# Optimization experiments

Hardware: AMD Instinct MI355X
Metric: run time of the kernel (lower is better)

## Reference

```python
import jax, jax.numpy as jnp
import numpy as np


def setup_inputs() -> dict:
    key = jax.random.key(0)
    X = jax.random.normal(key, (8, 64, 64, 64), dtype=jnp.float32)
    return {"X": X}


def reference(X):
    N, C, h, w = X.shape
    x1 = X.reshape(N, C, h * w)            # [N, C, HW]
    x2 = jnp.transpose(x1, (0, 2, 1))      # [N, HW, C]
    scores = jnp.einsum('bnc,bcm->bnm', x2, x1)  # [N, HW, HW]
    c = jax.nn.softmax(scores, axis=2)
    out = jnp.einsum('bnm,bmc->bnc', c, x2)      # [N, HW, C]
    out = jnp.transpose(out, (0, 2, 1)).reshape(N, C, h, w)
    return out
```

## Files before the change

### kernel.cpp

```cpp
#include <hip/hip_runtime.h>


#define SEQ 4096
#define DIM 64
#define LDB 72
#define LDP 72
#define LDO 68

typedef __attribute__((ext_vector_type(8))) short  short8;
typedef __attribute__((ext_vector_type(4))) float  f32x4;

__device__ __forceinline__ unsigned short f2bf(float f) {
    union { float f; unsigned int u; } x; x.f = f;
    unsigned int u = x.u + 0x7FFFu + ((x.u >> 16) & 1u);
    return (unsigned short)(u >> 16);
}
__device__ __forceinline__ float bf2f(unsigned short h) {
    union { unsigned int u; float f; } x; x.u = ((unsigned int)h) << 16; return x.f;
}

__global__ __launch_bounds__(256) void prepass2(const float* __restrict__ X,
                                                unsigned short* __restrict__ Xbf,
                                                unsigned short* __restrict__ XbfT,
                                                float* __restrict__ Norms,
                                                float* __restrict__ MaxNorm) {
    __shared__ float sN[16 * 65];
    const int b = blockIdx.y, m0 = blockIdx.x * 64;
    const float* Xb = X + (size_t)b * DIM * SEQ;
    unsigned short* Bb = Xbf  + (size_t)b * DIM * SEQ;
    unsigned short* Tb = XbfT + (size_t)b * SEQ * DIM;
    const int t = threadIdx.x, mw = t & 15, cg = t >> 4;

    unsigned short hb[4][4];
    #pragma unroll
    for (int cr = 0; cr < 4; ++cr) {
        const int c = cg * 4 + cr;
        const f32x4 v = *(const f32x4*)(Xb + (size_t)c * SEQ + m0 + mw * 4);
        hb[cr][0] = f2bf(v.x); hb[cr][1] = f2bf(v.y); hb[cr][2] = f2bf(v.z); hb[cr][3] = f2bf(v.w);
        *(ushort4*)(Bb + (size_t)c * SEQ + m0 + mw * 4) =
            make_ushort4(hb[cr][0], hb[cr][1], hb[cr][2], hb[cr][3]);
    }
    #pragma unroll
    for (int mr = 0; mr < 4; ++mr) {
        float nrm = 0.f;
        #pragma unroll
        for (int cr = 0; cr < 4; ++cr) { const float fv = bf2f(hb[cr][mr]); nrm += fv * fv; }
        *(ushort4*)(Tb + (size_t)(m0 + mw * 4 + mr) * DIM + cg * 4) =
            make_ushort4(hb[0][mr], hb[1][mr], hb[2][mr], hb[3][mr]);
        sN[cg * 65 + mw * 4 + mr] = nrm;
    }
    __syncthreads();
    if (t < 64) {
        float s = 0.f;
        #pragma unroll
        for (int i = 0; i < 16; ++i) s += sN[i * 65 + t];
        const float nm = sqrtf(s);
        Norms[(size_t)b * SEQ + m0 + t] = nm;
        float mx = nm;
        #pragma unroll
        for (int d = 1; d < 64; d <<= 1) mx = fmaxf(mx, __shfl_xor(mx, d));
        if (t == 0) atomicMax((unsigned int*)(MaxNorm + b), __float_as_uint(mx));
    }
}

__global__ __launch_bounds__(256, 2) void attn_main(const unsigned short* __restrict__ Xbf,
                                                    const unsigned short* __restrict__ XbfT,
                                                    const float* __restrict__ Norms,
                                                    const float* __restrict__ MaxNorm,
                                                    float* __restrict__ Out) {
    __shared__ __align__(16) unsigned char smem[16384 + 16384 + 4 * 16 * LDP * 2];
    unsigned short* sK = (unsigned short*)smem;
    unsigned short* sV = (unsigned short*)(smem + 16384);
    unsigned short* sP = (unsigned short*)(smem + 32768);
    float*          sO = (float*)smem;

    const int tid  = threadIdx.x;
    const int lane = tid & 63;
    const int w    = tid >> 6;
    const int l15  = lane & 15;
    const int quad = lane >> 4;

    const int b  = blockIdx.y;
    const int s0 = blockIdx.x * 64;
    const unsigned short* Bb = Xbf  + (size_t)b * DIM * SEQ;
    const unsigned short* Tb = XbfT + (size_t)b * SEQ * DIM;

    const unsigned short* qp = Tb + (size_t)(s0 + 16 * w + l15) * DIM + quad * 8;
    const short8 qf0 = *(const short8*)(qp);
    const short8 qf1 = *(const short8*)(qp + 32);

    const float mrow = Norms[(size_t)b * SEQ + s0 + 16 * w + l15] * MaxNorm[b];

    f32x4 acc_o[4];
    #pragma unroll
    for (int ct = 0; ct < 4; ++ct) acc_o[ct] = (f32x4){0.f, 0.f, 0.f, 0.f};
    float lpart = 0.f;
    unsigned short* sPw = sP + w * 16 * LDP;

    const int rl = lane >> 3, cgp = lane & 7;
    const int cgs = cgp ^ rl;
    auto stage = [&](int kt, int half) {
        unsigned short* sKb = sK + half * 4096;
        unsigned short* sVb = sV + half * 4096;
        #pragma unroll
        for (int j = 0; j < 2; ++j) {
            const int row = (2 * w + j) * 8 + rl;
            const unsigned short* gK = Tb + ((size_t)(kt * 64 + row) << 6) + (cgs << 3);
            const unsigned short* gV = Bb + (((size_t)row) << 12) + (kt << 6) + (cgs << 3);
            __builtin_amdgcn_global_load_lds(
                (const __attribute__((address_space(1))) unsigned int*)gK,
                (__attribute__((address_space(3))) unsigned int*)(sKb + ((2 * w + j) << 9)),
                16, 0, 0);
            __builtin_amdgcn_global_load_lds(
                (const __attribute__((address_space(1))) unsigned int*)gV,
                (__attribute__((address_space(3))) unsigned int*)(sVb + ((2 * w + j) << 9)),
                16, 0, 0);
        }
    };

    const int rsw = l15 & 7;
    auto compute = [&](int half) {
        const unsigned short* sKc = sK + half * 4096;
        const unsigned short* sVc = sV + half * 4096;
        short8 kf[2][4], vf[2][4];
        #pragma unroll
        for (int t4 = 0; t4 < 4; ++t4) {
            const int rowoff = (16 * t4 + l15) << 6;
            #pragma unroll
            for (int ks = 0; ks < 2; ++ks) {
                const int cgr = (((quad + 4 * ks) ^ rsw) << 3);
                kf[ks][t4] = *(const short8*)(sKc + rowoff + cgr);
                vf[ks][t4] = *(const short8*)(sVc + rowoff + cgr);
            }
        }
        #pragma unroll
        for (int mt = 0; mt < 4; ++mt) {
            f32x4 a = (f32x4){0.f, 0.f, 0.f, 0.f};
            a = __builtin_amdgcn_mfma_f32_16x16x32_bf16(kf[0][mt], qf0, a, 0, 0, 0);
            a = __builtin_amdgcn_mfma_f32_16x16x32_bf16(kf[1][mt], qf1, a, 0, 0, 0);
            const float p0 = __expf(a[0] - mrow);
            const float p1 = __expf(a[1] - mrow);
            const float p2 = __expf(a[2] - mrow);
            const float p3 = __expf(a[3] - mrow);
            lpart += (p0 + p1) + (p2 + p3);
            const unsigned u0 = __float_as_uint(p0) + 0x8000u;
            const unsigned u1 = __float_as_uint(p1) + 0x8000u;
            const unsigned u2 = __float_as_uint(p2) + 0x8000u;
            const unsigned u3 = __float_as_uint(p3) + 0x8000u;
            const unsigned lo = __builtin_amdgcn_perm(u1, u0, 0x07060302u);
            const unsigned hi = __builtin_amdgcn_perm(u3, u2, 0x07060302u);
            *(uint2*)(sPw + l15 * LDP + 16 * mt + quad * 4) = make_uint2(lo, hi);
        }
        const short8 pf0 = *(const short8*)(sPw + l15 * LDP + quad * 8);
        const short8 pf1 = *(const short8*)(sPw + l15 * LDP + 32 + quad * 8);
        #pragma unroll
        for (int ct = 0; ct < 4; ++ct) {
            acc_o[ct] = __builtin_amdgcn_mfma_f32_16x16x32_bf16(pf0, vf[0][ct], acc_o[ct], 0, 0, 0);
            acc_o[ct] = __builtin_amdgcn_mfma_f32_16x16x32_bf16(pf1, vf[1][ct], acc_o[ct], 0, 0, 0);
        }
    };

    stage(0, 0);
    __syncthreads();
    for (int kt = 0; kt < 64; kt += 2) {
        stage(kt + 1, 1);
        compute(0);
        __syncthreads();
        if (kt + 2 < 64) stage(kt + 2, 0);
        compute(1);
        __syncthreads();
    }

    lpart += __shfl_xor(lpart, 16);
    lpart += __shfl_xor(lpart, 32);
    float inv[4];
    #pragma unroll
    for (int r = 0; r < 4; ++r) inv[r] = 1.f / __shfl(lpart, 4 * quad + r);

    #pragma unroll
    for (int ct = 0; ct < 4; ++ct) {
        const int c = 16 * ct + l15;
        #pragma unroll
        for (int r = 0; r < 4; ++r)
            sO[c * LDO + 16 * w + quad * 4 + r] = acc_o[ct][r] * inv[r];
    }
    __syncthreads();
    const int mgrp = tid & 15, c0 = tid >> 4;
    #pragma unroll
    for (int cc = 0; cc < 4; ++cc) {
        const int c = c0 + 16 * cc;
        const f32x4 v = *(const f32x4*)(sO + c * LDO + 4 * mgrp);
        *(f32x4*)(Out + (size_t)b * DIM * SEQ + (size_t)c * SEQ + s0 + 4 * mgrp) = v;
    }
}

__global__ __launch_bounds__(256, 2) void attn_fallback(const float* __restrict__ X,
                                                        float* __restrict__ Out) {
    __shared__ __align__(16) unsigned char smem[27648];
    unsigned short* sK = (unsigned short*)smem;
    unsigned short* sV = (unsigned short*)(smem + 9216);
    unsigned short* sP = (unsigned short*)(smem + 18432);
    float*          sO = (float*)smem;

    const int tid  = threadIdx.x;
    const int lane = tid & 63;
    const int w    = tid >> 6;
    const int l15  = lane & 15;
    const int quad = lane >> 4;
    const int b  = blockIdx.y;
    const int s0 = blockIdx.x * 64;
    const float* Xb = X + (size_t)b * DIM * SEQ;
    const int mgrp = tid & 15;
    const int c0   = tid >> 4;

    for (int cc = 0; cc < 4; ++cc) {
        int c = c0 + 16 * cc;
        const f32x4 v = *(const f32x4*)(Xb + (size_t)c * SEQ + s0 + 4 * mgrp);
        sK[(4 * mgrp + 0) * LDB + c] = f2bf(v.x);
        sK[(4 * mgrp + 1) * LDB + c] = f2bf(v.y);
        sK[(4 * mgrp + 2) * LDB + c] = f2bf(v.z);
        sK[(4 * mgrp + 3) * LDB + c] = f2bf(v.w);
    }
    __syncthreads();
    short8 qf0, qf1;
    {
        const int row = 16 * w + l15;
        qf0 = *(const short8*)(sK + row * LDB + quad * 8);
        qf1 = *(const short8*)(sK + row * LDB + 32 + quad * 8);
    }
    __syncthreads();

    f32x4 acc_o[4];
    for (int ct = 0; ct < 4; ++ct) acc_o[ct] = (f32x4){0.f, 0.f, 0.f, 0.f};
    float m_i[4] = {-1e30f, -1e30f, -1e30f, -1e30f};
    float l_i[4] = {0.f, 0.f, 0.f, 0.f};

    for (int kt = 0; kt < SEQ / 64; ++kt) {
        const int m0 = kt * 64;
        for (int cc = 0; cc < 4; ++cc) {
            int c = c0 + 16 * cc;
            const f32x4 v = *(const f32x4*)(Xb + (size_t)c * SEQ + m0 + 4 * mgrp);
            unsigned short h0 = f2bf(v.x), h1 = f2bf(v.y), h2 = f2bf(v.z), h3 = f2bf(v.w);
            *(ushort4*)(sV + c * LDB + 4 * mgrp) = make_ushort4(h0, h1, h2, h3);
            sK[(4 * mgrp + 0) * LDB + c] = h0;
            sK[(4 * mgrp + 1) * LDB + c] = h1;
            sK[(4 * mgrp + 2) * LDB + c] = h2;
            sK[(4 * mgrp + 3) * LDB + c] = h3;
        }
        __syncthreads();

        short8 vf[2][4];
        for (int ks = 0; ks < 2; ++ks)
            for (int ct = 0; ct < 4; ++ct)
                vf[ks][ct] = *(const short8*)(sV + (16 * ct + l15) * LDB + ks * 32 + quad * 8);

        f32x4 acc_s[4];
        for (int mt = 0; mt < 4; ++mt) {
            const int row = 16 * mt + l15;
            const short8 kf0 = *(const short8*)(sK + row * LDB + quad * 8);
            const short8 kf1 = *(const short8*)(sK + row * LDB + 32 + quad * 8);
            f32x4 a = (f32x4){0.f, 0.f, 0.f, 0.f};
            a = __builtin_amdgcn_mfma_f32_16x16x32_bf16(qf0, kf0, a, 0, 0, 0);
            a = __builtin_amdgcn_mfma_f32_16x16x32_bf16(qf1, kf1, a, 0, 0, 0);
            acc_s[mt] = a;
        }

        float alpha[4];
        for (int r = 0; r < 4; ++r) {
            float mx = fmaxf(fmaxf(acc_s[0][r], acc_s[1][r]), fmaxf(acc_s[2][r], acc_s[3][r]));
            mx = fmaxf(mx, __shfl_xor(mx, 1));
            mx = fmaxf(mx, __shfl_xor(mx, 2));
            mx = fmaxf(mx, __shfl_xor(mx, 4));
            mx = fmaxf(mx, __shfl_xor(mx, 8));
            const float mnew = fmaxf(m_i[r], mx);
            alpha[r] = __expf(m_i[r] - mnew);
            m_i[r] = mnew;
        }
        float rowsum[4] = {0.f, 0.f, 0.f, 0.f};
        unsigned short pb[4][4];
        for (int mt = 0; mt < 4; ++mt)
            for (int r = 0; r < 4; ++r) {
                const float p = __expf(acc_s[mt][r] - m_i[r]);
                rowsum[r] += p;
                pb[mt][r] = f2bf(p);
            }
        for (int r = 0; r < 4; ++r) {
            float s = rowsum[r];
            s += __shfl_xor(s, 1);
            s += __shfl_xor(s, 2);
            s += __shfl_xor(s, 4);
            s += __shfl_xor(s, 8);
            l_i[r] = alpha[r] * l_i[r] + s;
        }
        for (int ct = 0; ct < 4; ++ct)
            for (int r = 0; r < 4; ++r)
                acc_o[ct][r] *= alpha[r];

        for (int mt = 0; mt < 4; ++mt)
            for (int r = 0; r < 4; ++r)
                sP[(16 * w + quad * 4 + r) * LDB + l15 + 16 * mt] = pb[mt][r];
        __syncthreads();

        const short8 pf0 = *(const short8*)(sP + (16 * w + l15) * LDB + quad * 8);
        const short8 pf1 = *(const short8*)(sP + (16 * w + l15) * LDB + 32 + quad * 8);
        for (int ct = 0; ct < 4; ++ct) {
            acc_o[ct] = __builtin_amdgcn_mfma_f32_16x16x32_bf16(pf0, vf[0][ct], acc_o[ct], 0, 0, 0);
            acc_o[ct] = __builtin_amdgcn_mfma_f32_16x16x32_bf16(pf1, vf[1][ct], acc_o[ct], 0, 0, 0);
        }
    }

    float inv[4];
    for (int r = 0; r < 4; ++r) inv[r] = 1.f / l_i[r];
    for (int ct = 0; ct < 4; ++ct) {
        const int c = 16 * ct + l15;
        for (int r = 0; r < 4; ++r)
            sO[c * LDO + 16 * w + quad * 4 + r] = acc_o[ct][r] * inv[r];
    }
    __syncthreads();
    for (int cc = 0; cc < 4; ++cc) {
        const int c = c0 + 16 * cc;
        const f32x4 v = *(const f32x4*)(sO + c * LDO + 4 * mgrp);
        *(f32x4*)(Out + (size_t)b * DIM * SEQ + (size_t)c * SEQ + s0 + 4 * mgrp) = v;
    }
}

extern "C" void kernel_launch(void* const* d_in, const int* in_sizes, int n_in,
                              void* d_out, int out_size, void* d_ws, size_t ws_size,
                              hipStream_t stream) {
    const float* X = (const float*)d_in[0];
    float* Out = (float*)d_out;
    const size_t elems = (size_t)8 * SEQ * DIM;
    const size_t need  = elems * 2 * 2 + (size_t)8 * SEQ * 4 + 8 * 4;
    if (ws_size >= need) {
        unsigned short* Xbf  = (unsigned short*)d_ws;
        unsigned short* XbfT = Xbf + elems;
        float* Norms   = (float*)(XbfT + elems);
        float* MaxNorm = Norms + (size_t)8 * SEQ;
        hipMemsetAsync(MaxNorm, 0, 8 * sizeof(float), stream);
        dim3 grid(64, 8);
        prepass2<<<grid, 256, 0, stream>>>(X, Xbf, XbfT, Norms, MaxNorm);
        attn_main<<<grid, 256, 0, stream>>>(Xbf, XbfT, Norms, MaxNorm, Out);
    } else {
        attn_fallback<<<dim3(64, 8), 256, 0, stream>>>(X, Out);
    }
}
```

Before: 124.7 us.

## Split key range across two blocks with combine pass, fold log2e into Q

Attention now splits the key sequence in half across a third grid dimension. Each half writes unnormalized partial outputs and row sums, and a new combine kernel adds them and divides. Blocks shrink to 128 threads, each wave handling two 16-row query tiles, which doubles K/V reuse per wave. The query copy is prescaled by log2(e) (sqrt per side) so the softmax can use exp2f. The prepass builds its transpose through LDS, and a per-block max array replaces the memset plus atomicMax. The cost is extra global traffic for partial outputs and an added kernel launch.

```diff
diff --git a/kernel.cpp b/kernel.cpp
--- a/kernel.cpp
+++ b/kernel.cpp
@@ -1,11 +1,12 @@
 #include <hip/hip_runtime.h>
+#include <math.h>
 
 
 #define SEQ 4096
 #define DIM 64
 #define LDB 72
-#define LDP 72
 #define LDO 68
+#define QSCALE 1.2011224087864498f
 
 typedef __attribute__((ext_vector_type(8))) short  short8;
 typedef __attribute__((ext_vector_type(4))) float  f32x4;
@@ -19,56 +20,68 @@
     union { unsigned int u; float f; } x; x.u = ((unsigned int)h) << 16; return x.f;
 }
 
-__global__ __launch_bounds__(256) void prepass2(const float* __restrict__ X,
+#define LDT 68
+__global__ __launch_bounds__(256) void prepass3(const float* __restrict__ X,
                                                 unsigned short* __restrict__ Xbf,
                                                 unsigned short* __restrict__ XbfT,
                                                 float* __restrict__ Norms,
-                                                float* __restrict__ MaxNorm) {
-    __shared__ float sN[16 * 65];
+                                                float* __restrict__ MaxPart) {
+    __shared__ __align__(16) unsigned short sT[64 * LDT];
+    __shared__ float sRed[4];
     const int b = blockIdx.y, m0 = blockIdx.x * 64;
     const float* Xb = X + (size_t)b * DIM * SEQ;
     unsigned short* Bb = Xbf  + (size_t)b * DIM * SEQ;
     unsigned short* Tb = XbfT + (size_t)b * SEQ * DIM;
-    const int t = threadIdx.x, mw = t & 15, cg = t >> 4;
-
-    unsigned short hb[4][4];
+    const int t = threadIdx.x, w = t >> 6;
+    const int mw = t & 15, cg = t >> 4;
+
     #pragma unroll
     for (int cr = 0; cr < 4; ++cr) {
         const int c = cg * 4 + cr;
-        const f32x4 v = *(const f32x4*)(Xb + (size_t)c * SEQ + m0 + mw * 4);
-        hb[cr][0] = f2bf(v.x); hb[cr][1] = f2bf(v.y); hb[cr][2] = f2bf(v.z); hb[cr][3] = f2bf(v.w);
-        *(ushort4*)(Bb + (size_t)c * SEQ + m0 + mw * 4) =
-            make_ushort4(hb[cr][0], hb[cr][1], hb[cr][2], hb[cr][3]);
-    }
-    #pragma unroll
-    for (int mr = 0; mr < 4; ++mr) {
-        float nrm = 0.f;
-        #pragma unroll
-        for (int cr = 0; cr < 4; ++cr) { const float fv = bf2f(hb[cr][mr]); nrm += fv * fv; }
-        *(ushort4*)(Tb + (size_t)(m0 + mw * 4 + mr) * DIM + cg * 4) =
-            make_ushort4(hb[0][mr], hb[1][mr], hb[2][mr], hb[3][mr]);
-        sN[cg * 65 + mw * 4 + mr] = nrm;
-    }
-    __syncthreads();
-    if (t < 64) {
-        float s = 0.f;
-        #pragma unroll
-        for (int i = 0; i < 16; ++i) s += sN[i * 65 + t];
-        const float nm = sqrtf(s);
-        Norms[(size_t)b * SEQ + m0 + t] = nm;
-        float mx = nm;
-        #pragma unroll
-        for (int d = 1; d < 64; d <<= 1) mx = fmaxf(mx, __shfl_xor(mx, d));
-        if (t == 0) atomicMax((unsigned int*)(MaxNorm + b), __float_as_uint(mx));
-    }
-}
-
-__global__ __launch_bounds__(256, 2) void attn_main(const unsigned short* __restrict__ Xbf,
-                                                    const unsigned short* __restrict__ XbfT,
-                                                    const float* __restrict__ Norms,
-                                                    const float* __restrict__ MaxNorm,
-                                                    float* __restrict__ Out) {
-    __shared__ __align__(16) unsigned char smem[16384 + 16384 + 4 * 16 * LDP * 2];
+        const f32x4 v = *(const f32x4*)(Xb + (size_t)c * SEQ + m0 + 4 * mw);
+        *(ushort4*)(Bb + (size_t)c * SEQ + m0 + 4 * mw) =
+            make_ushort4(f2bf(v.x), f2bf(v.y), f2bf(v.z), f2bf(v.w));
+        sT[(4 * mw + 0) * LDT + c] = f2bf(v.x * QSCALE);
+        sT[(4 * mw + 1) * LDT + c] = f2bf(v.y * QSCALE);
+        sT[(4 * mw + 2) * LDT + c] = f2bf(v.z * QSCALE);
+        sT[(4 * mw + 3) * LDT + c] = f2bf(v.w * QSCALE);
+    }
+    __syncthreads();
+    const int m = t >> 2, ck = t & 3;
+    const short8 a0 = *(const short8*)(sT + m * LDT + ck * 16);
+    const short8 a1 = *(const short8*)(sT + m * LDT + ck * 16 + 8);
+    *(short8*)(Tb + (size_t)(m0 + m) * DIM + ck * 16)     = a0;
+    *(short8*)(Tb + (size_t)(m0 + m) * DIM + ck * 16 + 8) = a1;
+    float s = 0.f;
+    #pragma unroll
+    for (int i = 0; i < 8; ++i) {
+        const float f0 = bf2f((unsigned short)a0[i]);
+        const float f1 = bf2f((unsigned short)a1[i]);
+        s += f0 * f0 + f1 * f1;
+    }
+    s += __shfl_xor(s, 1);
+    s += __shfl_xor(s, 2);
+    const float nm = sqrtf(s);
+    if (ck == 0) Norms[(size_t)b * SEQ + m0 + m] = nm;
+    float mx = nm;
+    #pragma unroll
+    for (int d = 4; d < 64; d <<= 1) mx = fmaxf(mx, __shfl_xor(mx, d));
+    if ((t & 63) == 0) sRed[w] = mx;
+    __syncthreads();
+    if (t == 0)
+        MaxPart[b * 64 + blockIdx.x] =
+            fmaxf(fmaxf(sRed[0], sRed[1]), fmaxf(sRed[2], sRed[3]));
+}
+
+template <bool PARTIAL>
+__global__ __launch_bounds__(128, 2) void attn_split(const unsigned short* __restrict__ Xbf,
+                                                     const unsigned short* __restrict__ XbfT,
+                                                     const float* __restrict__ Norms,
+                                                     const float* __restrict__ MaxPart,
+                                                     float* __restrict__ Obase,
+                                                     float* __restrict__ Lbase,
+                                                     int niter) {
+    __shared__ __align__(16) unsigned char smem[40960];
     unsigned short* sK = (unsigned short*)smem;
     unsigned short* sV = (unsigned short*)(smem + 16384);
     unsigned short* sP = (unsigned short*)(smem + 32768);
@@ -80,41 +93,60 @@
     const int l15  = lane & 15;
     const int quad = lane >> 4;
 
-    const int b  = blockIdx.y;
-    const int s0 = blockIdx.x * 64;
+    const int b   = blockIdx.y;
+    const int s0  = blockIdx.x * 64;
+    const int h   = blockIdx.z;
+    const int kt0 = h * niter;
     const unsigned short* Bb = Xbf  + (size_t)b * DIM * SEQ;
     const unsigned short* Tb = XbfT + (size_t)b * SEQ * DIM;
-
-    const unsigned short* qp = Tb + (size_t)(s0 + 16 * w + l15) * DIM + quad * 8;
-    const short8 qf0 = *(const short8*)(qp);
-    const short8 qf1 = *(const short8*)(qp + 32);
-
-    const float mrow = Norms[(size_t)b * SEQ + s0 + 16 * w + l15] * MaxNorm[b];
-
-    f32x4 acc_o[4];
-    #pragma unroll
-    for (int ct = 0; ct < 4; ++ct) acc_o[ct] = (f32x4){0.f, 0.f, 0.f, 0.f};
-    float lpart = 0.f;
-    unsigned short* sPw = sP + w * 16 * LDP;
-
-    const int rl = lane >> 3, cgp = lane & 7;
-    const int cgs = cgp ^ rl;
+    float* Optr = Obase + (size_t)h * 8 * DIM * SEQ;
+    float* Lptr = PARTIAL ? (Lbase + (size_t)h * 8 * SEQ) : nullptr;
+
+    float mxn = MaxPart[b * 64 + lane];
+    #pragma unroll
+    for (int d = 1; d < 64; d <<= 1) mxn = fmaxf(mxn, __shfl_xor(mxn, d));
+
+    short8 qf[2][2];
+    float mrow[2];
+    #pragma unroll
+    for (int qt = 0; qt < 2; ++qt) {
+        const int row = s0 + 32 * w + 16 * qt + l15;
+        const unsigned short* qp = Tb + (size_t)row * DIM + quad * 8;
+        qf[qt][0] = *(const short8*)(qp);
+        qf[qt][1] = *(const short8*)(qp + 32);
+        mrow[qt] = Norms[(size_t)b * SEQ + row] * mxn;
+    }
+
+    f32x4 acc_o[2][4];
+    #pragma unroll
+    for (int qt = 0; qt < 2; ++qt)
+        #pragma unroll
+        for (int ct = 0; ct < 4; ++ct) acc_o[qt][ct] = (f32x4){0.f, 0.f, 0.f, 0.f};
+    float lp[2] = {0.f, 0.f};
+    unsigned short* sPw = sP + w * 32 * 64;
+
+    const int rl = lane >> 3, cgs = (lane & 7) ^ rl;
+    int koff[4], voff[4], ldsoff[4];
+    #pragma unroll
+    for (int j = 0; j < 4; ++j) {
+        const int row_j = w * 8 + j * 16 + rl;
+        koff[j]   = row_j * 64 + cgs * 8;
+        voff[j]   = row_j * 4096 + cgs * 8;
+        ldsoff[j] = (w * 8 + j * 16) * 64;
+    }
     auto stage = [&](int kt, int half) {
         unsigned short* sKb = sK + half * 4096;
         unsigned short* sVb = sV + half * 4096;
         #pragma unroll
-        for (int j = 0; j < 2; ++j) {
-            const int row = (2 * w + j) * 8 + rl;
-            const unsigned short* gK = Tb + ((size_t)(kt * 64 + row) << 6) + (cgs << 3);
-            const unsigned short* gV = Bb + (((size_t)row) << 12) + (kt << 6) + (cgs << 3);
+        for (int j = 0; j < 4; ++j) {
+            const unsigned short* gK = Tb + (size_t)kt * 4096 + koff[j];
+            const unsigned short* gV = Bb + (size_t)kt * 64 + voff[j];
             __builtin_amdgcn_global_load_lds(
                 (const __attribute__((address_space(1))) unsigned int*)gK,
-                (__attribute__((address_space(3))) unsigned int*)(sKb + ((2 * w + j) << 9)),
-                16, 0, 0);
+                (__attribute__((address_space(3))) unsigned int*)(sKb + ldsoff[j]), 16, 0, 0);
             __builtin_amdgcn_global_load_lds(
                 (const __attribute__((address_space(1))) unsigned int*)gV,
-                (__attribute__((address_space(3))) unsigned int*)(sVb + ((2 * w + j) << 9)),
-                16, 0, 0);
+                (__attribute__((address_space(3))) unsigned int*)(sVb + ldsoff[j]), 16, 0, 0);
         }
     };
 
@@ -134,64 +166,109 @@
             }
         }
         #pragma unroll
-        for (int mt = 0; mt < 4; ++mt) {
-            f32x4 a = (f32x4){0.f, 0.f, 0.f, 0.f};
-            a = __builtin_amdgcn_mfma_f32_16x16x32_bf16(kf[0][mt], qf0, a, 0, 0, 0);
-            a = __builtin_amdgcn_mfma_f32_16x16x32_bf16(kf[1][mt], qf1, a, 0, 0, 0);
-            const float p0 = __expf(a[0] - mrow);
-            const float p1 = __expf(a[1] - mrow);
-            const float p2 = __expf(a[2] - mrow);
-            const float p3 = __expf(a[3] - mrow);
-            lpart += (p0 + p1) + (p2 + p3);
-            const unsigned u0 = __float_as_uint(p0) + 0x8000u;
-            const unsigned u1 = __float_as_uint(p1) + 0x8000u;
-            const unsigned u2 = __float_as_uint(p2) + 0x8000u;
-            const unsigned u3 = __float_as_uint(p3) + 0x8000u;
-            const unsigned lo = __builtin_amdgcn_perm(u1, u0, 0x07060302u);
-            const unsigned hi = __builtin_amdgcn_perm(u3, u2, 0x07060302u);
-            *(uint2*)(sPw + l15 * LDP + 16 * mt + quad * 4) = make_uint2(lo, hi);
-        }
-        const short8 pf0 = *(const short8*)(sPw + l15 * LDP + quad * 8);
-        const short8 pf1 = *(const short8*)(sPw + l15 * LDP + 32 + quad * 8);
-        #pragma unroll
-        for (int ct = 0; ct < 4; ++ct) {
-            acc_o[ct] = __builtin_amdgcn_mfma_f32_16x16x32_bf16(pf0, vf[0][ct], acc_o[ct], 0, 0, 0);
-            acc_o[ct] = __builtin_amdgcn_mfma_f32_16x16x32_bf16(pf1, vf[1][ct], acc_o[ct], 0, 0, 0);
+        for (int qt = 0; qt < 2; ++qt) {
+            const int nloc = 16 * qt + l15;
+            #pragma unroll
+            for (int mt = 0; mt < 4; ++mt) {
+                f32x4 a = (f32x4){0.f, 0.f, 0.f, 0.f};
+                a = __builtin_amdgcn_mfma_f32_16x16x32_bf16(kf[0][mt], qf[qt][0], a, 0, 0, 0);
+                a = __builtin_amdgcn_mfma_f32_16x16x32_bf16(kf[1][mt], qf[qt][1], a, 0, 0, 0);
+                const float p0 = exp2f(a[0] - mrow[qt]);
+                const float p1 = exp2f(a[1] - mrow[qt]);
+                const float p2 = exp2f(a[2] - mrow[qt]);
+                const float p3 = exp2f(a[3] - mrow[qt]);
+                lp[qt] += (p0 + p1) + (p2 + p3);
+                const unsigned u0 = __float_as_uint(p0) + 0x8000u;
+                const unsigned u1 = __float_as_uint(p1) + 0x8000u;
+                const unsigned u2 = __float_as_uint(p2) + 0x8000u;
+                const unsigned u3 = __float_as_uint(p3) + 0x8000u;
+                const unsigned lo = __builtin_amdgcn_perm(u1, u0, 0x07060302u);
+                const unsigned hi = __builtin_amdgcn_perm(u3, u2, 0x07060302u);
+                const int chk = (2 * mt + (quad >> 1)) ^ rsw;
+                *(uint2*)(sPw + nloc * 64 + chk * 8 + 4 * (quad & 1)) = make_uint2(lo, hi);
+            }
+            const short8 pf0 = *(const short8*)(sPw + nloc * 64 + ((quad)     ^ rsw) * 8);
+            const short8 pf1 = *(const short8*)(sPw + nloc * 64 + ((quad + 4) ^ rsw) * 8);
+            #pragma unroll
+            for (int ct = 0; ct < 4; ++ct) {
+                acc_o[qt][ct] = __builtin_amdgcn_mfma_f32_16x16x32_bf16(pf0, vf[0][ct], acc_o[qt][ct], 0, 0, 0);
+                acc_o[qt][ct] = __builtin_amdgcn_mfma_f32_16x16x32_bf16(pf1, vf[1][ct], acc_o[qt][ct], 0, 0, 0);
+            }
         }
     };
 
-    stage(0, 0);
-    __syncthreads();
-    for (int kt = 0; kt < 64; kt += 2) {
-        stage(kt + 1, 1);
+    stage(kt0, 0);
+    __syncthreads();
+    for (int it = 0; it < niter; it += 2) {
+        if (it + 1 < niter) stage(kt0 + it + 1, 1);
         compute(0);
         __syncthreads();
-        if (kt + 2 < 64) stage(kt + 2, 0);
+        if (it + 2 < niter) stage(kt0 + it + 2, 0);
         compute(1);
         __syncthreads();
     }
 
-    lpart += __shfl_xor(lpart, 16);
-    lpart += __shfl_xor(lpart, 32);
-    float inv[4];
-    #pragma unroll
-    for (int r = 0; r < 4; ++r) inv[r] = 1.f / __shfl(lpart, 4 * quad + r);
-
-    #pragma unroll
-    for (int ct = 0; ct < 4; ++ct) {
-        const int c = 16 * ct + l15;
-        #pragma unroll
-        for (int r = 0; r < 4; ++r)
-            sO[c * LDO + 16 * w + quad * 4 + r] = acc_o[ct][r] * inv[r];
-    }
-    __syncthreads();
-    const int mgrp = tid & 15, c0 = tid >> 4;
-    #pragma unroll
-    for (int cc = 0; cc < 4; ++cc) {
-        const int c = c0 + 16 * cc;
-        const f32x4 v = *(const f32x4*)(sO + c * LDO + 4 * mgrp);
-        *(f32x4*)(Out + (size_t)b * DIM * SEQ + (size_t)c * SEQ + s0 + 4 * mgrp) = v;
-    }
+    #pragma unroll
+    for (int qt = 0; qt < 2; ++qt) {
+        lp[qt] += __shfl_xor(lp[qt], 16);
+        lp[qt] += __shfl_xor(lp[qt], 32);
+    }
+
+    if (PARTIAL) {
+        if (quad == 0) {
+            #pragma unroll
+            for (int qt = 0; qt < 2; ++qt)
+                Lptr[(size_t)b * SEQ + s0 + 32 * w + 16 * qt + l15] = lp[qt];
+        }
+    } else {
+        #pragma unroll
+        for (int qt = 0; qt < 2; ++qt) {
+            float inv[4];
+            #pragma unroll
+            for (int r = 0; r < 4; ++r) inv[r] = 1.f / __shfl(lp[qt], 4 * quad + r);
+            #pragma unroll
+            for (int ct = 0; ct < 4; ++ct)
+                #pragma unroll
+                for (int r = 0; r < 4; ++r) acc_o[qt][ct][r] *= inv[r];
+        }
+    }
+
+    #pragma unroll
+    for (int qt = 0; qt < 2; ++qt)
+        #pragma unroll
+        for (int ct = 0; ct < 4; ++ct) {
+            const int c = 16 * ct + l15;
+            #pragma unroll
+            for (int r = 0; r < 4; ++r)
+                sO[c * LDO + 32 * w + 16 * qt + 4 * quad + r] = acc_o[qt][ct][r];
+        }
+    __syncthreads();
+    const int mw = tid & 15, cg = tid >> 4;
+    #pragma unroll
+    for (int cc = 0; cc < 8; ++cc) {
+        const int c = cg + 8 * cc;
+        const f32x4 v = *(const f32x4*)(sO + c * LDO + 4 * mw);
+        *(f32x4*)(Optr + ((size_t)b * DIM + c) * SEQ + s0 + 4 * mw) = v;
+    }
+}
+
+__global__ __launch_bounds__(256) void combine_kernel(const float* __restrict__ O0,
+                                                      const float* __restrict__ O1,
+                                                      const float* __restrict__ L0,
+                                                      const float* __restrict__ L1,
+                                                      float* __restrict__ Out) {
+    const int gid = blockIdx.x * 256 + threadIdx.x;
+    const size_t base = (size_t)gid * 4;
+    const int s = (int)(base & 4095);
+    const int b = (int)(base >> 18);
+    const f32x4 o0 = *(const f32x4*)(O0 + base);
+    const f32x4 o1 = *(const f32x4*)(O1 + base);
+    const f32x4 l0 = *(const f32x4*)(L0 + b * SEQ + s);
+    const f32x4 l1 = *(const f32x4*)(L1 + b * SEQ + s);
+    f32x4 o;
+    #pragma unroll
+    for (int i = 0; i < 4; ++i) o[i] = (o0[i] + o1[i]) / (l0[i] + l1[i]);
+    *(f32x4*)(Out + base) = o;
 }
 
 __global__ __launch_bounds__(256, 2) void attn_fallback(const float* __restrict__ X,
@@ -201,7 +278,6 @@
     unsigned short* sV = (unsigned short*)(smem + 9216);
     unsigned short* sP = (unsigned short*)(smem + 18432);
     float*          sO = (float*)smem;
-
     const int tid  = threadIdx.x;
     const int lane = tid & 63;
     const int w    = tid >> 6;
@@ -229,12 +305,10 @@
         qf1 = *(const short8*)(sK + row * LDB + 32 + quad * 8);
     }
     __syncthreads();
-
     f32x4 acc_o[4];
     for (int ct = 0; ct < 4; ++ct) acc_o[ct] = (f32x4){0.f, 0.f, 0.f, 0.f};
     float m_i[4] = {-1e30f, -1e30f, -1e30f, -1e30f};
     float l_i[4] = {0.f, 0.f, 0.f, 0.f};
-
     for (int kt = 0; kt < SEQ / 64; ++kt) {
         const int m0 = kt * 64;
         for (int cc = 0; cc < 4; ++cc) {
@@ -248,12 +322,10 @@
             sK[(4 * mgrp + 3) * LDB + c] = h3;
         }
         __syncthreads();
-
         short8 vf[2][4];
         for (int ks = 0; ks < 2; ++ks)
             for (int ct = 0; ct < 4; ++ct)
                 vf[ks][ct] = *(const short8*)(sV + (16 * ct + l15) * LDB + ks * 32 + quad * 8);
-
         f32x4 acc_s[4];
         for (int mt = 0; mt < 4; ++mt) {
             const int row = 16 * mt + l15;
@@ -264,7 +336,6 @@
             a = __builtin_amdgcn_mfma_f32_16x16x32_bf16(qf1, kf1, a, 0, 0, 0);
             acc_s[mt] = a;
         }
-
         float alpha[4];
         for (int r = 0; r < 4; ++r) {
             float mx = fmaxf(fmaxf(acc_s[0][r], acc_s[1][r]), fmaxf(acc_s[2][r], acc_s[3][r]));
@@ -295,12 +366,10 @@
         for (int ct = 0; ct < 4; ++ct)
             for (int r = 0; r < 4; ++r)
                 acc_o[ct][r] *= alpha[r];
-
         for (int mt = 0; mt < 4; ++mt)
             for (int r = 0; r < 4; ++r)
                 sP[(16 * w + quad * 4 + r) * LDB + l15 + 16 * mt] = pb[mt][r];
         __syncthreads();
-
         const short8 pf0 = *(const short8*)(sP + (16 * w + l15) * LDB + quad * 8);
         const short8 pf1 = *(const short8*)(sP + (16 * w + l15) * LDB + 32 + quad * 8);
         for (int ct = 0; ct < 4; ++ct) {
@@ -308,7 +377,6 @@
             acc_o[ct] = __builtin_amdgcn_mfma_f32_16x16x32_bf16(pf1, vf[1][ct], acc_o[ct], 0, 0, 0);
         }
     }
-
     float inv[4];
     for (int r = 0; r < 4; ++r) inv[r] = 1.f / l_i[r];
     for (int ct = 0; ct < 4; ++ct) {
@@ -330,16 +398,33 @@
     const float* X = (const float*)d_in[0];
     float* Out = (float*)d_out;
     const size_t elems = (size_t)8 * SEQ * DIM;
-    const size_t need  = elems * 2 * 2 + (size_t)8 * SEQ * 4 + 8 * 4;
-    if (ws_size >= need) {
-        unsigned short* Xbf  = (unsigned short*)d_ws;
-        unsigned short* XbfT = Xbf + elems;
-        float* Norms   = (float*)(XbfT + elems);
-        float* MaxNorm = Norms + (size_t)8 * SEQ;
-        hipMemsetAsync(MaxNorm, 0, 8 * sizeof(float), stream);
-        dim3 grid(64, 8);
-        prepass2<<<grid, 256, 0, stream>>>(X, Xbf, XbfT, Norms, MaxNorm);
-        attn_main<<<grid, 256, 0, stream>>>(Xbf, XbfT, Norms, MaxNorm, Out);
+    const size_t offXbfT  = elems * 2;
+    const size_t offNorms = offXbfT + elems * 2;
+    const size_t offMaxP  = offNorms + (size_t)8 * SEQ * 4;
+    const size_t offOpart = offMaxP + 8 * 64 * 4;
+    const size_t offLpart = offOpart + 2 * elems * 4;
+    const size_t need_split = offLpart + 2 * (size_t)8 * SEQ * 4;
+    const size_t need_h1    = offOpart;
+
+    if (ws_size >= need_h1) {
+        unsigned short* Xbf   = (unsigned short*)d_ws;
+        unsigned short* XbfT  = (unsigned short*)((char*)d_ws + offXbfT);
+        float* Norms   = (float*)((char*)d_ws + offNorms);
+        float* MaxPart = (float*)((char*)d_ws + offMaxP);
+        prepass3<<<dim3(64, 8), 256, 0, stream>>>(X, Xbf, XbfT, Norms, MaxPart);
+        if (ws_size >= need_split) {
+            float* O0 = (float*)((char*)d_ws + offOpart);
+            float* O1 = O0 + elems;
+            float* L0 = (float*)((char*)d_ws + offLpart);
+            float* L1 = L0 + (size_t)8 * SEQ;
+            attn_split<true><<<dim3(64, 8, 2), 128, 0, stream>>>(Xbf, XbfT, Norms, MaxPart,
+                                                                 O0, L0, 32);
+            const int ngrp = (int)(elems / 4 / 256);
+            combine_kernel<<<ngrp, 256, 0, stream>>>(O0, O1, L0, L1, Out);
+        } else {
+            attn_split<false><<<dim3(64, 8, 1), 128, 0, stream>>>(Xbf, XbfT, Norms, MaxPart,
+                                                                  Out, nullptr, 64);
+        }
     } else {
         attn_fallback<<<dim3(64, 8), 256, 0, stream>>>(X, Out);
     }
```

New measurement: 132.3 us. 6.1% more time.
